# Performance work log

Hardware: AMD Instinct MI355X
Metric: run time of the kernel (lower is better)

Reference implementation:

```python
import jax, jax.numpy as jnp
import numpy as np

N_NODES = 50000
N_EDGES = 1600000
D_IN = 128
D_OUT = 128


def setup_inputs() -> dict:
    key = jax.random.key(0)
    k1, k2, k3, k4, k5 = jax.random.split(key, 5)
    x = jax.random.normal(k1, (N_NODES, D_IN), dtype=jnp.float32)
    edge_index = jax.random.randint(k2, (2, N_EDGES), 0, N_NODES, dtype=jnp.int64)
    s = 1.0 / np.sqrt(D_IN)
    W_l = jax.random.normal(k3, (D_OUT, D_IN), dtype=jnp.float32) * s
    b_l = jax.random.normal(k4, (D_OUT,), dtype=jnp.float32) * s
    W_r = jax.random.normal(k5, (D_OUT, D_IN), dtype=jnp.float32) * s
    return {"x": x, "edge_index": edge_index, "W_l": W_l, "b_l": b_l, "W_r": W_r}


def reference(x, edge_index, W_l, b_l, W_r):
    src, dst = edge_index[0], edge_index[1]
    # mean aggregation of neighbor (source) features at destination nodes
    agg = jax.ops.segment_sum(x[src], dst, num_segments=N_NODES)  # [N, D_in]
    cnt = jax.ops.segment_sum(jnp.ones((src.shape[0],), dtype=x.dtype), dst,
                              num_segments=N_NODES)
    mean = agg / jnp.maximum(cnt, 1.0)[:, None]
    # SAGEConv: lin_l(mean_neighbors) + lin_r(x_root); bias only on lin_l
    out = mean @ W_l.T + b_l + x @ W_r.T
    # last=False, act=relu, dropout inactive (p=0.0 / eval mode)
    return jax.nn.relu(out)
```

## Files before the change

### kernel.cpp

```cpp
#include <hip/hip_runtime.h>
#include <hip/hip_bf16.h>

#define NN 50000
#define NE 1600000
#define D  128
#define NB   500
#define NPB  100
#define RCAP 4224
#define NBB  512
#define ECH  3125
#define CASTB 1024
#define FRONTG (NBB + CASTB + 8)
#define NGRP 7
#define PSTR 132

typedef unsigned int u32;
typedef unsigned long long u64;
typedef unsigned short u16;
typedef __attribute__((ext_vector_type(8))) short short8;
typedef __attribute__((ext_vector_type(4))) float f32x4;
typedef __attribute__((ext_vector_type(2))) float f32x2;

#define GCUR_OFF 0
#define REG_OFF  4096
#define XF8_OFF  8452096
#define XB_OFF   14852224
#define WB_OFF   27652224

__device__ __forceinline__ u32 pack2(float a, float b) {
    u32 ua = __float_as_uint(a), ub = __float_as_uint(b);
    ua = (ua + 0x7FFFu + ((ua >> 16) & 1u)) >> 16;
    ub = (ub + 0x7FFFu + ((ub >> 16) & 1u)) >> 16;
    return ua | (ub << 16);
}

__global__ __launch_bounds__(512) void k_front(const int* __restrict__ ei,
                                               const float* __restrict__ x,
                                               const float* __restrict__ Wl,
                                               const float* __restrict__ Wr,
                                               u32* __restrict__ gcur,
                                               u32* __restrict__ region,
                                               uint2* __restrict__ xf8,
                                               uint4* __restrict__ xb,
                                               uint4* __restrict__ Wb,
                                               u32* __restrict__ xzrow) {
    __shared__ u32 eL[ECH + 6];
    __shared__ u32 srt[ECH + 6];
    __shared__ u32 lh[512], sc[512], gb[512], lc[512];
    __shared__ u32 ps[256];

    const int bid = blockIdx.x;
    const int t = threadIdx.x;

    if (bid >= NBB + CASTB) {
        const int s = (bid - NBB - CASTB) * 512 + t;
        const int mat = s >> 11;
        const int j   = (s >> 4) & 127;
        const int k8  = (s & 15) * 8;
        const float* src = (mat ? Wr : Wl) + (size_t)j * 128 + k8;
        const float4 a = reinterpret_cast<const float4*>(src)[0];
        const float4 b = reinterpret_cast<const float4*>(src)[1];
        uint4 o;
        o.x = pack2(a.x, a.y); o.y = pack2(a.z, a.w);
        o.z = pack2(b.x, b.y); o.w = pack2(b.z, b.w);
        Wb[s] = o;
        if (s < 32) xzrow[s] = 0u;
        return;
    }

    if (bid >= NBB) {
        const int total = NN * D / 8;
        for (int i = (bid - NBB) * 512 + t; i < total; i += CASTB * 512) {
            const float4 a = reinterpret_cast<const float4*>(x)[2 * i];
            const float4 b = reinterpret_cast<const float4*>(x)[2 * i + 1];
            uint2 o8;
            o8.x = (u32)__builtin_amdgcn_cvt_pk_fp8_f32(a.z, a.w,
                     __builtin_amdgcn_cvt_pk_fp8_f32(a.x, a.y, 0, false), true);
            o8.y = (u32)__builtin_amdgcn_cvt_pk_fp8_f32(b.z, b.w,
                     __builtin_amdgcn_cvt_pk_fp8_f32(b.x, b.y, 0, false), true);
            xf8[i] = o8;
            uint4 ob;
            ob.x = pack2(a.x, a.y); ob.y = pack2(a.z, a.w);
            ob.z = pack2(b.x, b.y); ob.w = pack2(b.z, b.w);
            xb[i] = ob;
        }
        return;
    }

    const int lane = t & 63;
    const u64 zmask = __ballot((u32)ei[2 * lane + 1] == 0u);
    const bool is64 = (zmask == ~0ull);

    const int e0 = bid * ECH;

    lh[t] = 0u; lc[t] = 0u;
    __syncthreads();

    for (int i = t; i < ECH; i += 512) {
        const int e = e0 + i;
        int src, dst;
        if (is64) { src = ei[2 * (size_t)e]; dst = ei[2 * (size_t)(NE + e)]; }
        else      { src = ei[e];             dst = ei[NE + e]; }
        const u32 b2 = (u32)dst / NPB;
        const u32 dl = (u32)dst - b2 * NPB;
        eL[i] = (b2 << 23) | (dl << 16) | (u32)src;
        atomicAdd(&lh[b2], 1u);
    }
    __syncthreads();

    u32 a0 = 0u, a1 = 0u;
    if (t < 256) { a0 = lh[2 * t]; a1 = lh[2 * t + 1]; ps[t] = a0 + a1; }
    __syncthreads();
    for (int ofs = 1; ofs < 256; ofs <<= 1) {
        u32 v = 0u;
        if (t < 256 && t >= ofs) v = ps[t - ofs];
        __syncthreads();
        if (t < 256) ps[t] += v;
        __syncthreads();
    }
    if (t < 256) {
        const u32 base = ps[t] - (a0 + a1);
        sc[2 * t]     = base + a0;
        sc[2 * t + 1] = base + a0 + a1;
        if (a0) gb[2 * t]     = atomicAdd(&gcur[2 * t],     a0);
        if (a1) gb[2 * t + 1] = atomicAdd(&gcur[2 * t + 1], a1);
    }
    __syncthreads();

    for (int i = t; i < ECH; i += 512) {
        const u32 e = eL[i];
        const u32 b2 = e >> 23;
        const u32 lp = atomicAdd(&lc[b2], 1u);
        srt[(sc[b2] - lh[b2]) + lp] = e;
    }
    __syncthreads();

    for (int i = t; i < ECH; i += 512) {
        const u32 e    = srt[i];
        const u32 b2   = e >> 23;
        const u32 run0 = sc[b2] - lh[b2];
        const u32 pos  = gb[b2] + ((u32)i - run0);
        if (pos < RCAP) region[(size_t)b2 * RCAP + pos] = e;
    }
}

#define GLOAD(J) \
    const int  i##J = i + 2 * J + half; \
    const u32 ev##J = srt[i##J]; \
    const u32 sr##J = (i##J < s1) ? (ev##J & 0xFFFFu) : (u32)NN; \
    const u32 wv##J = xf8[(size_t)sr##J * 32 + q];

#define GACC(J) { \
    const f32x2 lo = __builtin_amdgcn_cvt_pk_f32_fp8((int)wv##J, false); \
    const f32x2 hi = __builtin_amdgcn_cvt_pk_f32_fp8((int)wv##J, true); \
    a01 += lo; a23 += hi; }

__global__ __launch_bounds__(1024, 8) void k_aggemm(const u32* __restrict__ xf8,
                                                    const u32* __restrict__ region,
                                                    const u32* __restrict__ gcur,
                                                    const uint4* __restrict__ xb,
                                                    const uint4* __restrict__ Wb,
                                                    const float* __restrict__ bl,
                                                    float* __restrict__ out) {
    __shared__ u32 ent[RCAP];
    __shared__ u32 srt[RCAP + 16];
    __shared__ u32 hist[128], segs[128], cur[128];
    __shared__ u16 As[16 * 256];
    __shared__ float part[2][16][PSTR];

    const int t = threadIdx.x;
    const int b = blockIdx.x;

    if (t < 128) { hist[t] = 0u; cur[t] = 0u; }
    __syncthreads();

    u32 cnt = gcur[b];
    if (cnt > RCAP) cnt = RCAP;
    const u32* reg = region + (size_t)b * RCAP;

    for (int i = t; i < (int)cnt; i += 1024) {
        const u32 e = reg[i];
        ent[i] = e;
        atomicAdd(&hist[(e >> 16) & 0x7Fu], 1u);
    }
    __syncthreads();

    if (t < 128) segs[t] = hist[t];
    __syncthreads();
    for (int ofs = 1; ofs < 128; ofs <<= 1) {
        u32 v = 0u;
        if (t < 128 && t >= ofs) v = segs[t - ofs];
        __syncthreads();
        if (t < 128) segs[t] += v;
        __syncthreads();
    }

    for (int i = t; i < (int)cnt; i += 1024) {
        const u32 e = ent[i];
        const u32 dl = (e >> 16) & 0x7Fu;
        const u32 p = (segs[dl] - hist[dl]) + atomicAdd(&cur[dl], 1u);
        srt[p] = e;
    }
    if (t < 16) srt[cnt + t] = (u32)NN;
    __syncthreads();

    const int w    = t >> 6;
    const int lane = t & 63;
    const int half = lane >> 5;
    const u32 q    = (u32)(lane & 31);
    const int m16  = lane & 15;
    const int kg   = lane >> 4;
    const int tc   = w & 7;
    const int kh   = w >> 3;
    const int row0 = b * NPB;

    const char* wbb = reinterpret_cast<const char*>(Wb) + kh * 32768
                    + (size_t)(tc * 16 + m16) * 256 + kg * 16;
    const short8 wf0 = *reinterpret_cast<const short8*>(wbb);
    const short8 wf1 = *reinterpret_cast<const short8*>(wbb + 64);
    const short8 wf2 = *reinterpret_cast<const short8*>(wbb + 128);
    const short8 wf3 = *reinterpret_cast<const short8*>(wbb + 192);
    const float bias = bl[tc * 16 + m16];

    const int sm   = t >> 4;
    const int slot = t & 15;
    const u32 byteX = ((u32)(sm * 512 + (128 + slot * 8) * 2)) ^ ((u32)(sm & 7) << 4);

    for (int g = 0; g < NGRP; ++g) {
        if (t < 256) {
            const int grow = g * 16 + sm;
            uint4 ox = {0u, 0u, 0u, 0u};
            if (grow < NPB) ox = xb[(size_t)(row0 + grow) * 16 + slot];
            *reinterpret_cast<uint4*>(reinterpret_cast<char*>(As) + byteX) = ox;
        }

        const int r = g * 16 + w;
        if (r < NPB) {
            const int deg = (int)hist[r];
            const int s1  = (int)segs[r];
            const int s0  = s1 - deg;

            f32x2 a01 = {0.f, 0.f}, a23 = {0.f, 0.f};
            for (int i = s0; i < s1; i += 16) {
                GLOAD(0) GLOAD(1) GLOAD(2) GLOAD(3)
                GLOAD(4) GLOAD(5) GLOAD(6) GLOAD(7)
                GACC(0) GACC(1) GACC(2) GACC(3)
                GACC(4) GACC(5) GACC(6) GACC(7)
            }

            const float r0 = a01.x + __shfl_xor(a01.x, 32);
            const float r1 = a01.y + __shfl_xor(a01.y, 32);
            const float r2 = a23.x + __shfl_xor(a23.x, 32);
            const float r3 = a23.y + __shfl_xor(a23.y, 32);

            if (lane < 32) {
                const float inv = deg ? 1.0f / (float)deg : 0.0f;
                uint2 o;
                o.x = pack2(r0 * inv, r1 * inv);
                o.y = pack2(r2 * inv, r3 * inv);
                const u32 byteM = ((u32)(w * 512 + q * 8)) ^ ((u32)(w & 7) << 4);
                *reinterpret_cast<uint2*>(reinterpret_cast<char*>(As) + byteM) = o;
            }
        }
        __syncthreads();

        f32x4 acc = {0.f, 0.f, 0.f, 0.f};
        {
            const int kbase = kh * 128;
            const u32 ab0 = ((u32)(m16 * 512 + (kbase +  0 + kg * 8) * 2)) ^ ((u32)(m16 & 7) << 4);
            const u32 ab1 = ((u32)(m16 * 512 + (kbase + 32 + kg * 8) * 2)) ^ ((u32)(m16 & 7) << 4);
            const u32 ab2 = ((u32)(m16 * 512 + (kbase + 64 + kg * 8) * 2)) ^ ((u32)(m16 & 7) << 4);
            const u32 ab3 = ((u32)(m16 * 512 + (kbase + 96 + kg * 8) * 2)) ^ ((u32)(m16 & 7) << 4);
            const short8 af0 = *reinterpret_cast<const short8*>(reinterpret_cast<const char*>(As) + ab0);
            const short8 af1 = *reinterpret_cast<const short8*>(reinterpret_cast<const char*>(As) + ab1);
            const short8 af2 = *reinterpret_cast<const short8*>(reinterpret_cast<const char*>(As) + ab2);
            const short8 af3 = *reinterpret_cast<const short8*>(reinterpret_cast<const char*>(As) + ab3);
            acc = __builtin_amdgcn_mfma_f32_16x16x32_bf16(af0, wf0, acc, 0, 0, 0);
            acc = __builtin_amdgcn_mfma_f32_16x16x32_bf16(af1, wf1, acc, 0, 0, 0);
            acc = __builtin_amdgcn_mfma_f32_16x16x32_bf16(af2, wf2, acc, 0, 0, 0);
            acc = __builtin_amdgcn_mfma_f32_16x16x32_bf16(af3, wf3, acc, 0, 0, 0);
        }

        if (kh == 1) {
            #pragma unroll
            for (int i = 0; i < 4; i++)
                part[g & 1][kg * 4 + i][tc * 16 + m16] = acc[i];
        }
        __syncthreads();

        if (kh == 0) {
            #pragma unroll
            for (int i = 0; i < 4; i++) {
                const int grow = g * 16 + kg * 4 + i;
                if (grow < NPB) {
                    const float s = acc[i] + part[g & 1][kg * 4 + i][tc * 16 + m16] + bias;
                    out[(size_t)(row0 + grow) * D + tc * 16 + m16] = fmaxf(s, 0.f);
                }
            }
        }
    }
}

extern "C" void kernel_launch(void* const* d_in, const int* in_sizes, int n_in,
                              void* d_out, int out_size, void* d_ws, size_t ws_size,
                              hipStream_t stream) {
    const float* x  = (const float*)d_in[0];
    const int*   ei = (const int*)  d_in[1];
    const float* Wl = (const float*)d_in[2];
    const float* bl = (const float*)d_in[3];
    const float* Wr = (const float*)d_in[4];

    char* ws = (char*)d_ws;
    u32*   gcur   = (u32*)(ws + GCUR_OFF);
    u32*   region = (u32*)(ws + REG_OFF);
    u32*   xf8    = (u32*)(ws + XF8_OFF);
    uint4* xb     = (uint4*)(ws + XB_OFF);
    uint4* Wb     = (uint4*)(ws + WB_OFF);
    float* out    = (float*)d_out;

    hipMemsetAsync(ws, 0, 4096, stream);
    k_front <<<FRONTG, 512, 0, stream>>>(ei, x, Wl, Wr, gcur, region,
                                         (uint2*)xf8, xb, Wb, xf8 + (size_t)NN * 32);
    k_aggemm<<<NB, 1024, 0, stream>>>(xf8, region, gcur, xb, Wb, bl, out);
}
```

Before: 82.74 us.

## Drop bf16 copy of x; convert root rows in GEMM kernel and use wave-shuffle scan

The front kernel no longer writes a bf16 copy of the whole node feature matrix. The aggregation/GEMM kernel instead reads fp32 x rows directly and packs them to bf16 when staging the root-term tile into shared memory. This removes a 12.8 MB write plus its later read, at the cost of twice the bytes on the per-block root-row loads. Separately, the 512-bin bucket prefix sum is rebuilt as a warp-shuffle scan plus a cross-wave combine, which cuts the many syncthreads barriers of the old shared-memory scan.

```diff
diff --git a/kernel.cpp b/kernel.cpp
--- a/kernel.cpp
+++ b/kernel.cpp
@@ -24,8 +24,7 @@
 #define GCUR_OFF 0
 #define REG_OFF  4096
 #define XF8_OFF  8452096
-#define XB_OFF   14852224
-#define WB_OFF   27652224
+#define WB_OFF   14852224
 
 __device__ __forceinline__ u32 pack2(float a, float b) {
     u32 ua = __float_as_uint(a), ub = __float_as_uint(b);
@@ -41,13 +40,12 @@
                                                u32* __restrict__ gcur,
                                                u32* __restrict__ region,
                                                uint2* __restrict__ xf8,
-                                               uint4* __restrict__ xb,
                                                uint4* __restrict__ Wb,
                                                u32* __restrict__ xzrow) {
     __shared__ u32 eL[ECH + 6];
     __shared__ u32 srt[ECH + 6];
     __shared__ u32 lh[512], sc[512], gb[512], lc[512];
-    __shared__ u32 ps[256];
+    __shared__ u32 wsum[8];
 
     const int bid = blockIdx.x;
     const int t = threadIdx.x;
@@ -79,10 +77,6 @@
             o8.y = (u32)__builtin_amdgcn_cvt_pk_fp8_f32(b.z, b.w,
                      __builtin_amdgcn_cvt_pk_fp8_f32(b.x, b.y, 0, false), true);
             xf8[i] = o8;
-            uint4 ob;
-            ob.x = pack2(a.x, a.y); ob.y = pack2(a.z, a.w);
-            ob.z = pack2(b.x, b.y); ob.w = pack2(b.z, b.w);
-            xb[i] = ob;
         }
         return;
     }
@@ -108,23 +102,21 @@
     }
     __syncthreads();
 
-    u32 a0 = 0u, a1 = 0u;
-    if (t < 256) { a0 = lh[2 * t]; a1 = lh[2 * t + 1]; ps[t] = a0 + a1; }
-    __syncthreads();
-    for (int ofs = 1; ofs < 256; ofs <<= 1) {
-        u32 v = 0u;
-        if (t < 256 && t >= ofs) v = ps[t - ofs];
-        __syncthreads();
-        if (t < 256) ps[t] += v;
-        __syncthreads();
-    }
-    if (t < 256) {
-        const u32 base = ps[t] - (a0 + a1);
-        sc[2 * t]     = base + a0;
-        sc[2 * t + 1] = base + a0 + a1;
-        if (a0) gb[2 * t]     = atomicAdd(&gcur[2 * t],     a0);
-        if (a1) gb[2 * t + 1] = atomicAdd(&gcur[2 * t + 1], a1);
-    }
+    const u32 orig = lh[t];
+    u32 v = orig;
+    #pragma unroll
+    for (int ofs = 1; ofs < 64; ofs <<= 1) {
+        const u32 n = __shfl_up(v, ofs, 64);
+        if (lane >= ofs) v += n;
+    }
+    if (lane == 63) wsum[t >> 6] = v;
+    __syncthreads();
+    u32 base = 0;
+    #pragma unroll
+    for (int ww = 0; ww < 8; ww++) base += (ww < (t >> 6)) ? wsum[ww] : 0u;
+    v += base;
+    sc[t] = v;
+    if (orig) gb[t] = atomicAdd(&gcur[t], orig);
     __syncthreads();
 
     for (int i = t; i < ECH; i += 512) {
@@ -158,7 +150,7 @@
 __global__ __launch_bounds__(1024, 8) void k_aggemm(const u32* __restrict__ xf8,
                                                     const u32* __restrict__ region,
                                                     const u32* __restrict__ gcur,
-                                                    const uint4* __restrict__ xb,
+                                                    const float* __restrict__ xf,
                                                     const uint4* __restrict__ Wb,
                                                     const float* __restrict__ bl,
                                                     float* __restrict__ out) {
@@ -229,9 +221,15 @@
     for (int g = 0; g < NGRP; ++g) {
         if (t < 256) {
             const int grow = g * 16 + sm;
-            uint4 ox = {0u, 0u, 0u, 0u};
-            if (grow < NPB) ox = xb[(size_t)(row0 + grow) * 16 + slot];
-            *reinterpret_cast<uint4*>(reinterpret_cast<char*>(As) + byteX) = ox;
+            uint4 o = {0u, 0u, 0u, 0u};
+            if (grow < NPB) {
+                const float* srcx = xf + (size_t)(row0 + grow) * D + slot * 8;
+                const float4 a = reinterpret_cast<const float4*>(srcx)[0];
+                const float4 bb = reinterpret_cast<const float4*>(srcx)[1];
+                o.x = pack2(a.x, a.y);  o.y = pack2(a.z, a.w);
+                o.z = pack2(bb.x, bb.y); o.w = pack2(bb.z, bb.w);
+            }
+            *reinterpret_cast<uint4*>(reinterpret_cast<char*>(As) + byteX) = o;
         }
 
         const int r = g * 16 + w;
@@ -314,12 +312,11 @@
     u32*   gcur   = (u32*)(ws + GCUR_OFF);
     u32*   region = (u32*)(ws + REG_OFF);
     u32*   xf8    = (u32*)(ws + XF8_OFF);
-    uint4* xb     = (uint4*)(ws + XB_OFF);
     uint4* Wb     = (uint4*)(ws + WB_OFF);
     float* out    = (float*)d_out;
 
     hipMemsetAsync(ws, 0, 4096, stream);
     k_front <<<FRONTG, 512, 0, stream>>>(ei, x, Wl, Wr, gcur, region,
-                                         (uint2*)xf8, xb, Wb, xf8 + (size_t)NN * 32);
-    k_aggemm<<<NB, 1024, 0, stream>>>(xf8, region, gcur, xb, Wb, bl, out);
+                                         (uint2*)xf8, Wb, xf8 + (size_t)NN * 32);
+    k_aggemm<<<NB, 1024, 0, stream>>>(xf8, region, gcur, x, Wb, bl, out);
 }
```

After: 72.54 us. 12.3% less time.
